# Optimization experiments

Hardware: AMD Instinct MI355X
Metric: run time of the kernel (lower is better)

## Reference

```python
import jax, jax.numpy as jnp
import numpy as np

TEMPERATURE = 0.07
NUM_HARD_NEGATIVES = 5
BATCH = 8192
DIM = 512
NUM_CLASSES = 512


def setup_inputs() -> dict:
    key = jax.random.key(0)
    k1, k2 = jax.random.split(key)
    features = jax.random.normal(k1, (BATCH, DIM), dtype=jnp.float32)
    indices = jax.random.randint(k2, (BATCH,), 0, NUM_CLASSES, dtype=jnp.int64)
    return {"features": features, "indices": indices}


def reference(features, indices):
    B = features.shape[0]
    neg_inf = jnp.float32(-jnp.inf)

    # L2 normalize (torch F.normalize: eps=1e-12 clamp on the norm)
    norm = jnp.linalg.norm(features, axis=1, keepdims=True)
    f = features / jnp.maximum(norm, 1e-12)

    # [B, B] cosine similarity
    sim = f @ f.T

    eye = jnp.eye(B, dtype=bool)

    # hard-negative mining: top-k off-diagonal similarities per row
    k = min(NUM_HARD_NEGATIVES, B - 2)
    topk_vals, _ = jax.lax.top_k(jnp.where(eye, neg_inf, sim), k)  # [B, k]
    hard_scores = topk_vals / TEMPERATURE
    # NOTE: original subtracts the GLOBAL max (scalar), faithfully reproduced
    exp_hard = jnp.exp(hard_scores - jnp.max(hard_scores))

    # positives: same index, excluding self
    pos_mask = (indices[:, None] == indices[None, :]) & ~eye  # [B, B] bool

    pos_scores = jnp.where(pos_mask, sim, neg_inf) / TEMPERATURE
    row_max = jnp.max(pos_scores, axis=1, keepdims=True)
    exp_pos = jnp.exp(pos_scores - row_max)

    denom = exp_pos.sum(axis=1, keepdims=True) + exp_hard.sum(axis=1, keepdims=True)
    log_probs = pos_scores - jnp.log(denom)

    # sum log-probs over positives, average per row by positive count
    num_pos = jnp.maximum(pos_mask.sum(axis=1), 1)
    per_sample = -jnp.where(pos_mask, log_probs, 0.0).sum(axis=1) / num_pos

    return per_sample.mean()  # reduction='mean'
```

## Files before the change

### kernel.cpp

```cpp
#include <hip/hip_runtime.h>

#define BN 8192
#define DIM 512
#define TEMP 0.07f
#define NPART 12
#define NEGINF (-__builtin_inff())

typedef _Float16 half8 __attribute__((ext_vector_type(8)));
typedef float f32x4 __attribute__((ext_vector_type(4)));

#define GLOAD16(gp, lp) __builtin_amdgcn_global_load_lds( \
    (__attribute__((address_space(1))) const void*)(gp),  \
    (__attribute__((address_space(3))) void*)(lp), 16, 0, 0)

__device__ __forceinline__ void ins5(float t5[5], float v) {
#pragma unroll
  for (int k = 0; k < 5; k++) {
    float old = t5[k];
    bool gt = v > old;
    t5[k] = gt ? v : old;
    v = gt ? old : v;
  }
}

__device__ __forceinline__ void lse_merge(float& m, float& s, float mp, float sp) {
  if (mp > m) {
    s = s * expf((m - mp) / TEMP) + sp;
    m = mp;
  } else if (sp > 0.f) {
    s += sp * expf((mp - m) / TEMP);
  }
}

__global__ __launch_bounds__(256) void k_normalize(const float* __restrict__ feat,
                                                   _Float16* __restrict__ f16,
                                                   unsigned* __restrict__ cells) {
  if (blockIdx.x == 0 && threadIdx.x == 0) {
    ((float*)cells)[1] = 0.0f;
    cells[2] = 0u;
  }
  int gid = blockIdx.x * 256 + threadIdx.x;
  int row = gid >> 6, lane = gid & 63;
  const float4* rp = (const float4*)(feat + (size_t)row * DIM);
  float4 v0 = rp[lane * 2];
  float4 v1 = rp[lane * 2 + 1];
  float ss = v0.x * v0.x + v0.y * v0.y + v0.z * v0.z + v0.w * v0.w +
             v1.x * v1.x + v1.y * v1.y + v1.z * v1.z + v1.w * v1.w;
#pragma unroll
  for (int m = 1; m < 64; m <<= 1) ss += __shfl_xor(ss, m, 64);
  float r = 1.0f / fmaxf(sqrtf(ss), 1e-12f);
  half8 o;
  o[0] = (_Float16)(v0.x * r); o[1] = (_Float16)(v0.y * r);
  o[2] = (_Float16)(v0.z * r); o[3] = (_Float16)(v0.w * r);
  o[4] = (_Float16)(v1.x * r); o[5] = (_Float16)(v1.y * r);
  o[6] = (_Float16)(v1.z * r); o[7] = (_Float16)(v1.w * r);
  ((half8*)(f16 + (size_t)row * DIM))[lane] = o;
}

__device__ __forceinline__ void store_rec(float* d, const float t5[5], float m, float s,
                                          float ps, float cn) {
  *(float4*)d = make_float4(t5[0], t5[1], t5[2], t5[3]);
  *(float4*)(d + 4) = make_float4(t5[4], m, s, ps);
  *(float4*)(d + 8) = make_float4(cn, 0.f, 0.f, 0.f);
}

__global__ __launch_bounds__(256, 3) void k_tri(const _Float16* __restrict__ f16,
                                                const int* __restrict__ idx,
                                                float* __restrict__ toppart) {
  __shared__ float Csm[64 * 129];
  _Float16* Asm = (_Float16*)Csm;
  _Float16* Bsm = Asm + 128 * 64;

  int t = threadIdx.x;
  int w = t >> 6, lane = t & 63;
  int wr = w >> 1, wc = w & 1;
  int l15 = lane & 15, l4 = lane >> 4;

  int b = blockIdx.x;
  int bi = (int)(64.5f - sqrtf(64.5f * 64.5f - 2.0f * (float)b));
  bi = bi < 0 ? 0 : (bi > 63 ? 63 : bi);
  while (bi > 0 && (bi * 64 - (bi * (bi - 1)) / 2) > b) bi--;
  while (((bi + 1) * 64 - ((bi + 1) * bi) / 2) <= b) bi++;
  int bj = bi + (b - (bi * 64 - (bi * (bi - 1)) / 2));
  bool diag = (bi == bj);

  int srow = t & 63;
  int sq = t >> 6;
  int growA = bi * 128 + srow;
  int growB = growA + 64;
  int ct = t & 127;
  int hh = t >> 7;
  int myA = idx[growA], myB = idx[growB], myC = idx[bj * 128 + ct];

  float t5a[5], t5b[5], t5c[5];
  float mA = NEGINF, sA = 0.f, psA = 0.f, cnA = 0.f;
  float mB = NEGINF, sB = 0.f, psB = 0.f, cnB = 0.f;
  float mC = NEGINF, sC = 0.f, psC = 0.f, cnC = 0.f;
#pragma unroll
  for (int k = 0; k < 5; k++) { t5a[k] = NEGINF; t5b[k] = NEGINF; t5c[k] = NEGINF; }

  int swz = l15 & 7;
  int jbase = bj * 128;
  f32x4 acc[4][4] = {};

  const _Float16* gA[4];
  const _Float16* gB[4];
  int ldsu[4];
#pragma unroll
  for (int p = 0; p < 4; p++) {
    int u = p * 256 + t;
    int row = u >> 3;
    int cko = (u & 7) ^ (row & 7);
    gA[p] = f16 + (size_t)(bi * 128 + row) * DIM + cko * 8;
    gB[p] = f16 + (size_t)(jbase + row) * DIM + cko * 8;
    ldsu[p] = u * 8;
  }

  for (int kc = 0; kc < 8; kc++) {
    int k0 = kc * 64;
    __syncthreads();
#pragma unroll
    for (int p = 0; p < 4; p++) {
      GLOAD16(gA[p] + k0, Asm + ldsu[p]);
      GLOAD16(gB[p] + k0, Bsm + ldsu[p]);
    }
    __syncthreads();
#pragma unroll
    for (int s = 0; s < 2; s++) {
      half8 af[4], bf[4];
#pragma unroll
      for (int ti = 0; ti < 4; ti++) {
        int row = wr * 64 + ti * 16 + l15;
        af[ti] = *(const half8*)(Asm + (row * 8 + ((s * 4 + l4) ^ swz)) * 8);
      }
#pragma unroll
      for (int tj = 0; tj < 4; tj++) {
        int row = wc * 64 + tj * 16 + l15;
        bf[tj] = *(const half8*)(Bsm + (row * 8 + ((s * 4 + l4) ^ swz)) * 8);
      }
#pragma unroll
      for (int ti = 0; ti < 4; ti++)
#pragma unroll
        for (int tj = 0; tj < 4; tj++)
          acc[ti][tj] = __builtin_amdgcn_mfma_f32_16x16x32_f16(af[ti], bf[tj], acc[ti][tj], 0, 0, 0);
    }
  }

  unsigned mMA = 0, mMB = 0;
  {
    const int4* ip = (const int4*)(idx + jbase + sq * 32);
#pragma unroll
    for (int q = 0; q < 8; q++) {
      int4 cv = ip[q];
      mMA |= ((unsigned)(cv.x == myA) << (q * 4)) | ((unsigned)(cv.y == myA) << (q * 4 + 1)) |
             ((unsigned)(cv.z == myA) << (q * 4 + 2)) | ((unsigned)(cv.w == myA) << (q * 4 + 3));
      mMB |= ((unsigned)(cv.x == myB) << (q * 4)) | ((unsigned)(cv.y == myB) << (q * 4 + 1)) |
             ((unsigned)(cv.z == myB) << (q * 4 + 2)) | ((unsigned)(cv.w == myB) << (q * 4 + 3));
    }
  }
  unsigned long long mC0 = 0, mC1 = 0;
  if (!diag) {
    const int4* ip = (const int4*)(idx + bi * 128);
#pragma unroll
    for (int q = 0; q < 16; q++) {
      int4 cv = ip[q];
      unsigned long long bits = (unsigned long long)((unsigned)(cv.x == myC) |
          ((unsigned)(cv.y == myC) << 1) | ((unsigned)(cv.z == myC) << 2) |
          ((unsigned)(cv.w == myC) << 3));
      mC0 |= bits << (q * 4);
    }
#pragma unroll
    for (int q = 16; q < 32; q++) {
      int4 cv = ip[q];
      unsigned long long bits = (unsigned long long)((unsigned)(cv.x == myC) |
          ((unsigned)(cv.y == myC) << 1) | ((unsigned)(cv.z == myC) << 2) |
          ((unsigned)(cv.w == myC) << 3));
      mC1 |= bits << ((q - 16) * 4);
    }
  }

  auto dump = [&]() {
#pragma unroll
    for (int ti = 0; ti < 4; ti++) {
      int r0 = ti * 16 + l4 * 4;
#pragma unroll
      for (int tj = 0; tj < 4; tj++) {
        int c = wc * 64 + tj * 16 + l15;
#pragma unroll
        for (int reg = 0; reg < 4; reg++)
          Csm[(r0 + reg) * 129 + c] = acc[ti][tj][reg];
      }
    }
  };
  auto scan_i = [&](float (&t5)[5], float& m, float& s, float& ps, float& cn,
                    int grow, unsigned match) {
    const float* rowp = Csm + srow * 129 + sq * 32;
    int gc0 = jbase + sq * 32;
#pragma unroll
    for (int it = 0; it < 8; it++) {
      float v0 = rowp[it * 4 + 0], v1 = rowp[it * 4 + 1];
      float v2 = rowp[it * 4 + 2], v3 = rowp[it * 4 + 3];
      unsigned m4 = (match >> (it * 4)) & 0xFu;
      float mx = fmaxf(fmaxf(v0, v1), fmaxf(v2, v3));
      if (mx > t5[4] || m4) {
        int gc = gc0 + it * 4;
        float vv[4] = {v0, v1, v2, v3};
#pragma unroll
        for (int e = 0; e < 4; e++) {
          bool notself = (gc + e != grow);
          if (((m4 >> e) & 1u) && notself) {
            float v = vv[e];
            float nm = fmaxf(m, v);
            s = s * expf((m - nm) / TEMP) + expf((v - nm) / TEMP);
            m = nm;
            ps += v;
            cn += 1.f;
          }
          if (vv[e] > t5[4] && notself) ins5(t5, vv[e]);
        }
      }
    }
  };
  auto scan_j = [&](unsigned long long mfull) {
    const float* cp = Csm + ct;
    unsigned match = (unsigned)(mfull >> (hh * 32));
#pragma unroll
    for (int it = 0; it < 8; it++) {
      int r = hh * 32 + it * 4;
      float v0 = cp[(r + 0) * 129], v1 = cp[(r + 1) * 129];
      float v2 = cp[(r + 2) * 129], v3 = cp[(r + 3) * 129];
      unsigned m4 = (match >> (it * 4)) & 0xFu;
      float mx = fmaxf(fmaxf(v0, v1), fmaxf(v2, v3));
      if (mx > t5c[4] || m4) {
        float vv[4] = {v0, v1, v2, v3};
#pragma unroll
        for (int e = 0; e < 4; e++) {
          if ((m4 >> e) & 1u) {
            float v = vv[e];
            float nm = fmaxf(mC, v);
            sC = sC * expf((mC - nm) / TEMP) + expf((v - nm) / TEMP);
            mC = nm;
            psC += v;
            cnC += 1.f;
          }
          if (vv[e] > t5c[4]) ins5(t5c, vv[e]);
        }
      }
    }
  };

  __syncthreads();
  if (wr == 0) dump();
  __syncthreads();
  scan_i(t5a, mA, sA, psA, cnA, growA, mMA);
  if (!diag) scan_j(mC0);
  __syncthreads();
  if (wr == 1) dump();
  __syncthreads();
  scan_i(t5b, mB, sB, psB, cnB, growB, mMB);
  if (!diag) scan_j(mC1);

  __syncthreads();
  {
    float* slotA = Csm + (size_t)(sq * 128 + srow) * 9;
    float* slotB = Csm + (size_t)(sq * 128 + 64 + srow) * 9;
#pragma unroll
    for (int k = 0; k < 5; k++) { slotA[k] = t5a[k]; slotB[k] = t5b[k]; }
    slotA[5] = mA; slotA[6] = sA; slotA[7] = psA; slotA[8] = cnA;
    slotB[5] = mB; slotB[6] = sB; slotB[7] = psB; slotB[8] = cnB;
    if (!diag) {
      float* sc = Csm + 4608 + (size_t)(hh * 128 + ct) * 9;
#pragma unroll
      for (int k = 0; k < 5; k++) sc[k] = t5c[k];
      sc[5] = mC; sc[6] = sC; sc[7] = psC; sc[8] = cnC;
    }
  }
  __syncthreads();
  if (t < 128) {
    float t5[5];
    float m = NEGINF, s = 0.f, ps = 0.f, cn = 0.f;
#pragma unroll
    for (int k = 0; k < 5; k++) t5[k] = NEGINF;
#pragma unroll
    for (int q = 0; q < 4; q++) {
      const float* s9 = Csm + (size_t)(q * 128 + t) * 9;
      for (int k = 0; k < 5; k++) {
        float v = s9[k];
        if (!(v > t5[4])) break;
        ins5(t5, v);
      }
      lse_merge(m, s, s9[5], s9[6]);
      ps += s9[7];
      cn += s9[8];
    }
    store_rec(toppart + ((size_t)(bi * 128 + t) * 64 + bj) * 12, t5, m, s, ps, cn);
  } else if (!diag) {
    int c = t - 128;
    float t5[5];
    float m = NEGINF, s = 0.f, ps = 0.f, cn = 0.f;
#pragma unroll
    for (int k = 0; k < 5; k++) t5[k] = NEGINF;
#pragma unroll
    for (int h = 0; h < 2; h++) {
      const float* s9 = Csm + 4608 + (size_t)(h * 128 + c) * 9;
      for (int k = 0; k < 5; k++) {
        float v = s9[k];
        if (!(v > t5[4])) break;
        ins5(t5, v);
      }
      lse_merge(m, s, s9[5], s9[6]);
      ps += s9[7];
      cn += s9[8];
    }
    store_rec(toppart + ((size_t)(bj * 128 + c) * 64 + bi) * 12, t5, m, s, ps, cn);
  }
}

__global__ __launch_bounds__(256, 3) void k_gemm_fb(const _Float16* __restrict__ f16,
                                                    const int* __restrict__ idx,
                                                    float* __restrict__ toppart) {
  __shared__ float Csm[64 * 129];
  _Float16* Asm = (_Float16*)Csm;
  _Float16* Bsm = Asm + 128 * 64;
  int t = threadIdx.x;
  int w = t >> 6, lane = t & 63;
  int wr = w >> 1, wc = w & 1;
  int l15 = lane & 15, l4 = lane >> 4;
  int b = blockIdx.x;
  int part = b % NPART;
  int bi = b / NPART;
  int startp = part < 4 ? part * 6 : 24 + (part - 4) * 5;
  int cntp = part < 4 ? 6 : 5;
  int srow = t & 63, sq = t >> 6;
  int growA = bi * 128 + srow, growB = growA + 64;
  int myA = idx[growA], myB = idx[growB];
  float t5a[5], t5b[5];
  float mA = NEGINF, sA = 0.f, psA = 0.f, cnA = 0.f;
  float mB = NEGINF, sB = 0.f, psB = 0.f, cnB = 0.f;
#pragma unroll
  for (int k = 0; k < 5; k++) { t5a[k] = NEGINF; t5b[k] = NEGINF; }
  int swz = l15 & 7;
  for (int jj = 0; jj < cntp; jj++) {
    int jbase = (startp + jj) * 128;
    f32x4 acc[4][4] = {};
    for (int kc = 0; kc < 8; kc++) {
      int k0 = kc * 64;
      __syncthreads();
#pragma unroll
      for (int p = 0; p < 4; p++) {
        int u = p * 256 + t;
        int row = u >> 3;
        int cko = (u & 7) ^ (row & 7);
        GLOAD16(f16 + (size_t)(bi * 128 + row) * DIM + k0 + cko * 8, Asm + u * 8);
        GLOAD16(f16 + (size_t)(jbase + row) * DIM + k0 + cko * 8, Bsm + u * 8);
      }
      __syncthreads();
#pragma unroll
      for (int s = 0; s < 2; s++) {
        half8 af[4], bf[4];
#pragma unroll
        for (int ti = 0; ti < 4; ti++) {
          int row = wr * 64 + ti * 16 + l15;
          af[ti] = *(const half8*)(Asm + (row * 8 + ((s * 4 + l4) ^ swz)) * 8);
        }
#pragma unroll
        for (int tj = 0; tj < 4; tj++) {
          int row = wc * 64 + tj * 16 + l15;
          bf[tj] = *(const half8*)(Bsm + (row * 8 + ((s * 4 + l4) ^ swz)) * 8);
        }
#pragma unroll
        for (int ti = 0; ti < 4; ti++)
#pragma unroll
          for (int tj = 0; tj < 4; tj++)
            acc[ti][tj] = __builtin_amdgcn_mfma_f32_16x16x32_f16(af[ti], bf[tj], acc[ti][tj], 0, 0, 0);
      }
    }
    unsigned mMA = 0, mMB = 0;
    {
      const int4* ip = (const int4*)(idx + jbase + sq * 32);
#pragma unroll
      for (int q = 0; q < 8; q++) {
        int4 cv = ip[q];
        mMA |= ((unsigned)(cv.x == myA) << (q * 4)) | ((unsigned)(cv.y == myA) << (q * 4 + 1)) |
               ((unsigned)(cv.z == myA) << (q * 4 + 2)) | ((unsigned)(cv.w == myA) << (q * 4 + 3));
        mMB |= ((unsigned)(cv.x == myB) << (q * 4)) | ((unsigned)(cv.y == myB) << (q * 4 + 1)) |
               ((unsigned)(cv.z == myB) << (q * 4 + 2)) | ((unsigned)(cv.w == myB) << (q * 4 + 3));
      }
    }
    auto dump = [&]() {
#pragma unroll
      for (int ti = 0; ti < 4; ti++) {
        int r0 = ti * 16 + l4 * 4;
#pragma unroll
        for (int tj = 0; tj < 4; tj++) {
          int c = wc * 64 + tj * 16 + l15;
#pragma unroll
          for (int reg = 0; reg < 4; reg++)
            Csm[(r0 + reg) * 129 + c] = acc[ti][tj][reg];
        }
      }
    };
    auto scan = [&](float (&t5)[5], float& m, float& s, float& ps, float& cn,
                    int grow, unsigned match) {
      const float* rowp = Csm + srow * 129 + sq * 32;
      int gc0 = jbase + sq * 32;
#pragma unroll
      for (int it = 0; it < 8; it++) {
        float v0 = rowp[it * 4 + 0], v1 = rowp[it * 4 + 1];
        float v2 = rowp[it * 4 + 2], v3 = rowp[it * 4 + 3];
        unsigned m4 = (match >> (it * 4)) & 0xFu;
        float mx = fmaxf(fmaxf(v0, v1), fmaxf(v2, v3));
        if (mx > t5[4] || m4) {
          int gc = gc0 + it * 4;
          float vv[4] = {v0, v1, v2, v3};
#pragma unroll
          for (int e = 0; e < 4; e++) {
            bool notself = (gc + e != grow);
            if (((m4 >> e) & 1u) && notself) {
              float v = vv[e];
              float nm = fmaxf(m, v);
              s = s * expf((m - nm) / TEMP) + expf((v - nm) / TEMP);
              m = nm;
              ps += v;
              cn += 1.f;
            }
            if (vv[e] > t5[4] && notself) ins5(t5, vv[e]);
          }
        }
      }
    };
    __syncthreads();
    if (wr == 0) dump();
    __syncthreads();
    scan(t5a, mA, sA, psA, cnA, growA, mMA);
    __syncthreads();
    if (wr == 1) dump();
    __syncthreads();
    scan(t5b, mB, sB, psB, cnB, growB, mMB);
  }
  __syncthreads();
  {
    float* slotA = Csm + (size_t)(sq * 128 + srow) * 9;
    float* slotB = Csm + (size_t)(sq * 128 + 64 + srow) * 9;
#pragma unroll
    for (int k = 0; k < 5; k++) { slotA[k] = t5a[k]; slotB[k] = t5b[k]; }
    slotA[5] = mA; slotA[6] = sA; slotA[7] = psA; slotA[8] = cnA;
    slotB[5] = mB; slotB[6] = sB; slotB[7] = psB; slotB[8] = cnB;
  }
  __syncthreads();
  if (t < 128) {
    float t5[5];
    float m = NEGINF, s = 0.f, ps = 0.f, cn = 0.f;
#pragma unroll
    for (int k = 0; k < 5; k++) t5[k] = NEGINF;
#pragma unroll
    for (int q = 0; q < 4; q++) {
      const float* s9 = Csm + (size_t)(q * 128 + t) * 9;
      for (int k = 0; k < 5; k++) {
        float v = s9[k];
        if (!(v > t5[4])) break;
        ins5(t5, v);
      }
      lse_merge(m, s, s9[5], s9[6]);
      ps += s9[7];
      cn += s9[8];
    }
    store_rec(toppart + ((size_t)(bi * 128 + t) * NPART + part) * 12, t5, m, s, ps, cn);
  }
}

__global__ __launch_bounds__(256) void k_merge(const float* __restrict__ toppart,
                                               float* __restrict__ merged,
                                               float* __restrict__ bmax, int nslots) {
  __shared__ float red[4];
  int t = threadIdx.x;
  int lane = t & 63, w = t >> 6;
  int row = blockIdx.x * 4 + w;

  float t5[5], m, s, ps, cn;
  if (lane < nslots) {
    const float* r12 = toppart + ((size_t)row * nslots + lane) * 12;
    float4 a = *(const float4*)r12;
    float4 bq = *(const float4*)(r12 + 4);
    float4 cq = *(const float4*)(r12 + 8);
    t5[0] = a.x; t5[1] = a.y; t5[2] = a.z; t5[3] = a.w; t5[4] = bq.x;
    m = bq.y; s = bq.z; ps = bq.w; cn = cq.x;
  } else {
    t5[0] = t5[1] = t5[2] = t5[3] = t5[4] = NEGINF;
    m = NEGINF; s = 0.f; ps = 0.f; cn = 0.f;
  }
#pragma unroll
  for (int off = 32; off > 0; off >>= 1) {
    float tp[5];
#pragma unroll
    for (int k = 0; k < 5; k++) tp[k] = __shfl_xor(t5[k], off, 64);
    float mp = __shfl_xor(m, off, 64), sp = __shfl_xor(s, off, 64);
    float pp = __shfl_xor(ps, off, 64), cp = __shfl_xor(cn, off, 64);
#pragma unroll
    for (int k = 0; k < 5; k++)
      if (tp[k] > t5[4]) ins5(t5, tp[k]);
    lse_merge(m, s, mp, sp);
    ps += pp;
    cn += cp;
  }
  if (lane == 0) {
    float* d = merged + (size_t)row * 8;
    *(float4*)d = make_float4(t5[0], t5[1], t5[2], t5[3]);
    *(float4*)(d + 4) = make_float4(t5[4], s, ps, cn);
    red[w] = t5[0];
  }
  __syncthreads();
  if (t == 0) bmax[blockIdx.x] = fmaxf(fmaxf(red[0], red[1]), fmaxf(red[2], red[3]));
}

__global__ __launch_bounds__(256) void k_final(const float* __restrict__ merged,
                                               const float* __restrict__ bmax, int nb,
                                               unsigned* __restrict__ cells,
                                               float* __restrict__ out) {
  __shared__ float red[256];
  int t = threadIdx.x;
  float mg = NEGINF;
  for (int i = t; i < nb; i += 256) mg = fmaxf(mg, bmax[i]);
  red[t] = mg;
  __syncthreads();
  for (int o = 128; o > 0; o >>= 1) {
    if (t < o) red[t] = fmaxf(red[t], red[t + o]);
    __syncthreads();
  }
  float Mg = red[0];
  __syncthreads();

  int row = blockIdx.x * 256 + t;
  const float* m8 = merged + (size_t)row * 8;
  float4 a = *(const float4*)m8;
  float4 bq = *(const float4*)(m8 + 4);
  float h = expf((a.x - Mg) / TEMP) + expf((a.y - Mg) / TEMP) + expf((a.z - Mg) / TEMP) +
            expf((a.w - Mg) / TEMP) + expf((bq.x - Mg) / TEMP);
  float s = bq.y, ps = bq.z, cn = bq.w;
  float v = 0.f;
  if (cn > 0.f) v = logf(s + h) - (ps / cn) / TEMP;
  red[t] = v;
  __syncthreads();
  for (int o = 128; o > 0; o >>= 1) {
    if (t < o) red[t] += red[t + o];
    __syncthreads();
  }
  if (t == 0) {
    atomicAdd((float*)cells + 1, red[0]);
    __threadfence();
    unsigned done = atomicAdd(&cells[2], 1u);
    if (done == gridDim.x - 1) {
      float total = atomicAdd((float*)cells + 1, 0.0f);
      out[0] = total * (1.0f / (float)BN);
    }
  }
}

extern "C" void kernel_launch(void* const* d_in, const int* in_sizes, int n_in,
                              void* d_out, int out_size, void* d_ws, size_t ws_size,
                              hipStream_t stream) {
  const float* feat = (const float*)d_in[0];
  const int* idx = (const int*)d_in[1];
  float* out = (float*)d_out;
  char* ws = (char*)d_ws;

  _Float16* f16 = (_Float16*)ws;
  const size_t F16B = (size_t)8 * 1024 * 1024;

  const size_t TRI_TOP = F16B;
  const size_t TRI_MERGED = TRI_TOP + (size_t)BN * 64 * 12 * 4;
  const size_t TRI_BMAX = TRI_MERGED + (size_t)BN * 8 * 4;
  const size_t TRI_CELLS = TRI_BMAX + (size_t)(BN / 4) * 4;
  const size_t TRI_NEED = TRI_CELLS + 64;

  if (ws_size >= TRI_NEED) {
    float* toppart = (float*)(ws + TRI_TOP);
    float* merged = (float*)(ws + TRI_MERGED);
    float* bmax = (float*)(ws + TRI_BMAX);
    unsigned* cells = (unsigned*)(ws + TRI_CELLS);
    k_normalize<<<dim3(BN / 4), dim3(256), 0, stream>>>(feat, f16, cells);
    k_tri<<<dim3(2080), dim3(256), 0, stream>>>(f16, idx, toppart);
    k_merge<<<dim3(BN / 4), dim3(256), 0, stream>>>(toppart, merged, bmax, 64);
    k_final<<<dim3(BN / 256), dim3(256), 0, stream>>>(merged, bmax, BN / 4, cells, out);
  } else {
    const size_t FB_TOP = F16B;
    const size_t FB_MERGED = FB_TOP + (size_t)BN * NPART * 12 * 4;
    const size_t FB_BMAX = FB_MERGED + (size_t)BN * 8 * 4;
    const size_t FB_CELLS = FB_BMAX + (size_t)(BN / 4) * 4;
    float* toppart = (float*)(ws + FB_TOP);
    float* merged = (float*)(ws + FB_MERGED);
    float* bmax = (float*)(ws + FB_BMAX);
    unsigned* cells = (unsigned*)(ws + FB_CELLS);
    k_normalize<<<dim3(BN / 4), dim3(256), 0, stream>>>(feat, f16, cells);
    k_gemm_fb<<<dim3((BN / 128) * NPART), dim3(256), 0, stream>>>(f16, idx, toppart);
    k_merge<<<dim3(BN / 4), dim3(256), 0, stream>>>(toppart, merged, bmax, NPART);
    k_final<<<dim3(BN / 256), dim3(256), 0, stream>>>(merged, bmax, BN / 4, cells, out);
  }
}
```

Before: 198.7 us.

## Fuse merge and final kernels, branchless top-5 scan, raise k_tri occupancy

Merges k_merge and k_final into one kernel in which the last block, found via an atomic counter, computes the global max and the loss sum, saving one launch. In k_tri, diagonal self-similarities are masked to -inf when written to shared memory and removed from the positive bitmasks, so the per-element notself checks go away. The top-5 insertion becomes an unconditional min/max network applied to every value rather than a thresholded branch. Launch bounds go from 3 to 4 waves per SIMD, which may force register spills, and the serial final reduction in a single block adds tail latency.

```diff
diff --git a/kernel.cpp b/kernel.cpp
--- a/kernel.cpp
+++ b/kernel.cpp
@@ -16,10 +16,9 @@
 __device__ __forceinline__ void ins5(float t5[5], float v) {
 #pragma unroll
   for (int k = 0; k < 5; k++) {
-    float old = t5[k];
-    bool gt = v > old;
-    t5[k] = gt ? v : old;
-    v = gt ? old : v;
+    float hi = fmaxf(t5[k], v);
+    v = fminf(t5[k], v);
+    t5[k] = hi;
   }
 }
 
@@ -36,7 +35,6 @@
                                                    _Float16* __restrict__ f16,
                                                    unsigned* __restrict__ cells) {
   if (blockIdx.x == 0 && threadIdx.x == 0) {
-    ((float*)cells)[1] = 0.0f;
     cells[2] = 0u;
   }
   int gid = blockIdx.x * 256 + threadIdx.x;
@@ -64,7 +62,7 @@
   *(float4*)(d + 8) = make_float4(cn, 0.f, 0.f, 0.f);
 }
 
-__global__ __launch_bounds__(256, 3) void k_tri(const _Float16* __restrict__ f16,
+__global__ __launch_bounds__(256, 4) void k_tri(const _Float16* __restrict__ f16,
                                                 const int* __restrict__ idx,
                                                 float* __restrict__ toppart) {
   __shared__ float Csm[64 * 129];
@@ -84,21 +82,6 @@
   int bj = bi + (b - (bi * 64 - (bi * (bi - 1)) / 2));
   bool diag = (bi == bj);
 
-  int srow = t & 63;
-  int sq = t >> 6;
-  int growA = bi * 128 + srow;
-  int growB = growA + 64;
-  int ct = t & 127;
-  int hh = t >> 7;
-  int myA = idx[growA], myB = idx[growB], myC = idx[bj * 128 + ct];
-
-  float t5a[5], t5b[5], t5c[5];
-  float mA = NEGINF, sA = 0.f, psA = 0.f, cnA = 0.f;
-  float mB = NEGINF, sB = 0.f, psB = 0.f, cnB = 0.f;
-  float mC = NEGINF, sC = 0.f, psC = 0.f, cnC = 0.f;
-#pragma unroll
-  for (int k = 0; k < 5; k++) { t5a[k] = NEGINF; t5b[k] = NEGINF; t5c[k] = NEGINF; }
-
   int swz = l15 & 7;
   int jbase = bj * 128;
   f32x4 acc[4][4] = {};
@@ -146,6 +129,21 @@
     }
   }
 
+  int srow = t & 63;
+  int sq = t >> 6;
+  int growA = bi * 128 + srow;
+  int growB = growA + 64;
+  int ct = t & 127;
+  int hh = t >> 7;
+  int myA = idx[growA], myB = idx[growB], myC = idx[jbase + ct];
+
+  float t5a[5], t5b[5], t5c[5];
+  float mA = NEGINF, sA = 0.f, psA = 0.f, cnA = 0.f;
+  float mB = NEGINF, sB = 0.f, psB = 0.f, cnB = 0.f;
+  float mC = NEGINF, sC = 0.f, psC = 0.f, cnC = 0.f;
+#pragma unroll
+  for (int k = 0; k < 5; k++) { t5a[k] = NEGINF; t5b[k] = NEGINF; t5c[k] = NEGINF; }
+
   unsigned mMA = 0, mMB = 0;
   {
     const int4* ip = (const int4*)(idx + jbase + sq * 32);
@@ -158,6 +156,12 @@
              ((unsigned)(cv.z == myB) << (q * 4 + 2)) | ((unsigned)(cv.w == myB) << (q * 4 + 3));
     }
   }
+  if (diag) {
+    unsigned dA = (unsigned)(srow - sq * 32);
+    if (dA < 32u) mMA &= ~(1u << dA);
+    unsigned dB = (unsigned)(64 + srow - sq * 32);
+    if (dB < 32u) mMB &= ~(1u << dB);
+  }
   unsigned long long mC0 = 0, mC1 = 0;
   if (!diag) {
     const int4* ip = (const int4*)(idx + bi * 128);
@@ -187,28 +191,28 @@
       for (int tj = 0; tj < 4; tj++) {
         int c = wc * 64 + tj * 16 + l15;
 #pragma unroll
-        for (int reg = 0; reg < 4; reg++)
-          Csm[(r0 + reg) * 129 + c] = acc[ti][tj][reg];
+        for (int reg = 0; reg < 4; reg++) {
+          float val = acc[ti][tj][reg];
+          if (diag && c == wr * 64 + r0 + reg) val = NEGINF;
+          Csm[(r0 + reg) * 129 + c] = val;
+        }
       }
     }
   };
   auto scan_i = [&](float (&t5)[5], float& m, float& s, float& ps, float& cn,
-                    int grow, unsigned match) {
+                    unsigned match) {
     const float* rowp = Csm + srow * 129 + sq * 32;
-    int gc0 = jbase + sq * 32;
 #pragma unroll
     for (int it = 0; it < 8; it++) {
       float v0 = rowp[it * 4 + 0], v1 = rowp[it * 4 + 1];
       float v2 = rowp[it * 4 + 2], v3 = rowp[it * 4 + 3];
+      ins5(t5, v0); ins5(t5, v1); ins5(t5, v2); ins5(t5, v3);
       unsigned m4 = (match >> (it * 4)) & 0xFu;
-      float mx = fmaxf(fmaxf(v0, v1), fmaxf(v2, v3));
-      if (mx > t5[4] || m4) {
-        int gc = gc0 + it * 4;
+      if (m4) {
         float vv[4] = {v0, v1, v2, v3};
 #pragma unroll
         for (int e = 0; e < 4; e++) {
-          bool notself = (gc + e != grow);
-          if (((m4 >> e) & 1u) && notself) {
+          if ((m4 >> e) & 1u) {
             float v = vv[e];
             float nm = fmaxf(m, v);
             s = s * expf((m - nm) / TEMP) + expf((v - nm) / TEMP);
@@ -216,7 +220,6 @@
             ps += v;
             cn += 1.f;
           }
-          if (vv[e] > t5[4] && notself) ins5(t5, vv[e]);
         }
       }
     }
@@ -229,9 +232,9 @@
       int r = hh * 32 + it * 4;
       float v0 = cp[(r + 0) * 129], v1 = cp[(r + 1) * 129];
       float v2 = cp[(r + 2) * 129], v3 = cp[(r + 3) * 129];
+      ins5(t5c, v0); ins5(t5c, v1); ins5(t5c, v2); ins5(t5c, v3);
       unsigned m4 = (match >> (it * 4)) & 0xFu;
-      float mx = fmaxf(fmaxf(v0, v1), fmaxf(v2, v3));
-      if (mx > t5c[4] || m4) {
+      if (m4) {
         float vv[4] = {v0, v1, v2, v3};
 #pragma unroll
         for (int e = 0; e < 4; e++) {
@@ -243,7 +246,6 @@
             psC += v;
             cnC += 1.f;
           }
-          if (vv[e] > t5c[4]) ins5(t5c, vv[e]);
         }
       }
     }
@@ -252,12 +254,12 @@
   __syncthreads();
   if (wr == 0) dump();
   __syncthreads();
-  scan_i(t5a, mA, sA, psA, cnA, growA, mMA);
+  scan_i(t5a, mA, sA, psA, cnA, mMA);
   if (!diag) scan_j(mC0);
   __syncthreads();
   if (wr == 1) dump();
   __syncthreads();
-  scan_i(t5b, mB, sB, psB, cnB, growB, mMB);
+  scan_i(t5b, mB, sB, psB, cnB, mMB);
   if (!diag) scan_j(mC1);
 
   __syncthreads();
@@ -312,7 +314,7 @@
       ps += s9[7];
       cn += s9[8];
     }
-    store_rec(toppart + ((size_t)(bj * 128 + c) * 64 + bi) * 12, t5, m, s, ps, cn);
+    store_rec(toppart + ((size_t)(jbase + c) * 64 + bi) * 12, t5, m, s, ps, cn);
   }
 }
 
@@ -469,10 +471,14 @@
   }
 }
 
-__global__ __launch_bounds__(256) void k_merge(const float* __restrict__ toppart,
-                                               float* __restrict__ merged,
-                                               float* __restrict__ bmax, int nslots) {
-  __shared__ float red[4];
+__global__ __launch_bounds__(256) void k_merge_final(const float* __restrict__ toppart,
+                                                     float* __restrict__ merged,
+                                                     float* __restrict__ bmax,
+                                                     unsigned* __restrict__ cells,
+                                                     float* __restrict__ out, int nslots) {
+  __shared__ float red[256];
+  __shared__ float wmax[4];
+  __shared__ int lastflag;
   int t = threadIdx.x;
   int lane = t & 63, w = t >> 6;
   int row = blockIdx.x * 4 + w;
@@ -507,18 +513,20 @@
     float* d = merged + (size_t)row * 8;
     *(float4*)d = make_float4(t5[0], t5[1], t5[2], t5[3]);
     *(float4*)(d + 4) = make_float4(t5[4], s, ps, cn);
-    red[w] = t5[0];
-  }
-  __syncthreads();
-  if (t == 0) bmax[blockIdx.x] = fmaxf(fmaxf(red[0], red[1]), fmaxf(red[2], red[3]));
-}
-
-__global__ __launch_bounds__(256) void k_final(const float* __restrict__ merged,
-                                               const float* __restrict__ bmax, int nb,
-                                               unsigned* __restrict__ cells,
-                                               float* __restrict__ out) {
-  __shared__ float red[256];
-  int t = threadIdx.x;
+    wmax[w] = t5[0];
+  }
+  __syncthreads();
+  if (t == 0) {
+    bmax[blockIdx.x] = fmaxf(fmaxf(wmax[0], wmax[1]), fmaxf(wmax[2], wmax[3]));
+    __threadfence();
+    unsigned done = atomicAdd(&cells[2], 1u);
+    lastflag = (done == gridDim.x - 1);
+  }
+  __syncthreads();
+  if (!lastflag) return;
+  __threadfence();
+
+  int nb = gridDim.x;
   float mg = NEGINF;
   for (int i = t; i < nb; i += 256) mg = fmaxf(mg, bmax[i]);
   red[t] = mg;
@@ -529,31 +537,23 @@
   }
   float Mg = red[0];
   __syncthreads();
-
-  int row = blockIdx.x * 256 + t;
-  const float* m8 = merged + (size_t)row * 8;
-  float4 a = *(const float4*)m8;
-  float4 bq = *(const float4*)(m8 + 4);
-  float h = expf((a.x - Mg) / TEMP) + expf((a.y - Mg) / TEMP) + expf((a.z - Mg) / TEMP) +
-            expf((a.w - Mg) / TEMP) + expf((bq.x - Mg) / TEMP);
-  float s = bq.y, ps = bq.z, cn = bq.w;
-  float v = 0.f;
-  if (cn > 0.f) v = logf(s + h) - (ps / cn) / TEMP;
-  red[t] = v;
+  float sum = 0.f;
+  for (int r = t; r < BN; r += 256) {
+    const float* m8 = merged + (size_t)r * 8;
+    float4 a = *(const float4*)m8;
+    float4 bq = *(const float4*)(m8 + 4);
+    float h = expf((a.x - Mg) / TEMP) + expf((a.y - Mg) / TEMP) + expf((a.z - Mg) / TEMP) +
+              expf((a.w - Mg) / TEMP) + expf((bq.x - Mg) / TEMP);
+    float ss = bq.y, pp = bq.z, cc = bq.w;
+    if (cc > 0.f) sum += logf(ss + h) - (pp / cc) / TEMP;
+  }
+  red[t] = sum;
   __syncthreads();
   for (int o = 128; o > 0; o >>= 1) {
     if (t < o) red[t] += red[t + o];
     __syncthreads();
   }
-  if (t == 0) {
-    atomicAdd((float*)cells + 1, red[0]);
-    __threadfence();
-    unsigned done = atomicAdd(&cells[2], 1u);
-    if (done == gridDim.x - 1) {
-      float total = atomicAdd((float*)cells + 1, 0.0f);
-      out[0] = total * (1.0f / (float)BN);
-    }
-  }
+  if (t == 0) out[0] = red[0] * (1.0f / (float)BN);
 }
 
 extern "C" void kernel_launch(void* const* d_in, const int* in_sizes, int n_in,
@@ -580,8 +580,7 @@
     unsigned* cells = (unsigned*)(ws + TRI_CELLS);
     k_normalize<<<dim3(BN / 4), dim3(256), 0, stream>>>(feat, f16, cells);
     k_tri<<<dim3(2080), dim3(256), 0, stream>>>(f16, idx, toppart);
-    k_merge<<<dim3(BN / 4), dim3(256), 0, stream>>>(toppart, merged, bmax, 64);
-    k_final<<<dim3(BN / 256), dim3(256), 0, stream>>>(merged, bmax, BN / 4, cells, out);
+    k_merge_final<<<dim3(BN / 4), dim3(256), 0, stream>>>(toppart, merged, bmax, cells, out, 64);
   } else {
     const size_t FB_TOP = F16B;
     const size_t FB_MERGED = FB_TOP + (size_t)BN * NPART * 12 * 4;
@@ -593,7 +592,6 @@
     unsigned* cells = (unsigned*)(ws + FB_CELLS);
     k_normalize<<<dim3(BN / 4), dim3(256), 0, stream>>>(feat, f16, cells);
     k_gemm_fb<<<dim3((BN / 128) * NPART), dim3(256), 0, stream>>>(f16, idx, toppart);
-    k_merge<<<dim3(BN / 4), dim3(256), 0, stream>>>(toppart, merged, bmax, NPART);
-    k_final<<<dim3(BN / 256), dim3(256), 0, stream>>>(merged, bmax, BN / 4, cells, out);
-  }
-}
+    k_merge_final<<<dim3(BN / 4), dim3(256), 0, stream>>>(toppart, merged, bmax, cells, out, NPART);
+  }
+}
```

New measurement: 263.4 us. +32.6%, slower.
